# Kernel optimization log

Measured on AMD Instinct MI355X. Metric: run time of the kernel, lower is better.

Reference implementation:

```python
import jax, jax.numpy as jnp
import numpy as np

B, T, E, U, H = 1024, 200, 64, 64, 4  # batch, hist_len, embed, num_units, head_num
NEG = -2.0**32 + 1  # padding value from the TF code
EPS = 1e-9


def setup_inputs() -> dict:
    key = jax.random.key(0)
    k1, k2, k3, k4 = jax.random.split(key, 4)
    input_info = jax.random.normal(k1, (B, T, E), dtype=jnp.float32)
    keys_length = jax.random.randint(k2, (B, 1), 1, T + 1)  # valid lengths in [1, T]
    W = jax.random.truncated_normal(k3, -2.0, 2.0, (E, 3 * U), dtype=jnp.float32) * 0.05
    W_output = jax.random.truncated_normal(k4, -2.0, 2.0, (U, U), dtype=jnp.float32) * 0.05
    gamma = jnp.ones((U,), dtype=jnp.float32)
    beta = jnp.zeros((U,), dtype=jnp.float32)
    return {"input_info": input_info, "keys_length": keys_length,
            "W": W, "W_output": W_output, "gamma": gamma, "beta": beta}


def reference(input_info, keys_length, W, W_output, gamma, beta):
    b, t, e = input_info.shape
    u = W_output.shape[0]
    dh = u // H  # per-head dim; TF scales by sqrt of this (post-split dim)
    qkv = input_info @ W                     # [B,T,3U]
    q, k, v = jnp.split(qkv, 3, axis=-1)     # each [B,T,U]
    q = q.reshape(b, t, H, dh)
    k = k.reshape(b, t, H, dh)
    v = v.reshape(b, t, H, dh)
    scores = jnp.einsum('bqhd,bkhd->bhqk', q, k) / jnp.sqrt(jnp.float32(dh))
    mask = jnp.arange(t)[None, :] < keys_length          # [B,T] key mask
    scores = jnp.where(mask[:, None, None, :], scores, jnp.float32(NEG))
    align = jax.nn.softmax(scores, axis=-1)              # [B,H,T,T]
    out = jnp.einsum('bhqk,bkhd->bqhd', align, v).reshape(b, t, u)
    out = out @ W_output                                 # output projection
    out = out + input_info                               # residual (dropout off at inference)
    mean = out.mean(axis=-1, keepdims=True)
    var = jnp.mean((out - mean) ** 2, axis=-1, keepdims=True)
    out = (out - mean) / jnp.sqrt(var + EPS) * gamma + beta  # layernorm
    return out
```

## Files before the change

### kernel.cpp

```cpp
#include <hip/hip_runtime.h>

#define B_  1024
#define T_  200
#define E_  64
#define U_  64
#define H_  4

typedef float f32x4   __attribute__((ext_vector_type(4)));
typedef float f32x16  __attribute__((ext_vector_type(16)));
typedef short bf16x8  __attribute__((ext_vector_type(8)));
typedef unsigned uint2v __attribute__((ext_vector_type(2)));

static __device__ __forceinline__ float bf2f(unsigned short u) {
  return __uint_as_float(((unsigned)u) << 16);
}
static __device__ __forceinline__ float ldf(const void* p, long i, bool bf) {
  return bf ? bf2f(reinterpret_cast<const unsigned short*>(p)[i])
            : reinterpret_cast<const float*>(p)[i];
}
static __device__ __forceinline__ unsigned pkbf2(float lo, float hi) {
  unsigned r;
  asm("v_cvt_pk_bf16_f32 %0, %1, %2" : "=v"(r) : "v"(lo), "v"(hi));
  return r;
}
static __device__ __forceinline__ void swap32(unsigned& a, unsigned& b) {
#if defined(__has_builtin) && __has_builtin(__builtin_amdgcn_permlane32_swap)
  uint2v r = __builtin_amdgcn_permlane32_swap(a, b, false, false);
  a = r[0]; b = r[1];
#else
  asm volatile("v_permlane32_swap_b32 %0, %1" : "+v"(a), "+v"(b));
#endif
}

#define QK_IDX(t, c) ((((t) << 4) + (c)) ^ ((((t) >> 2) & 1) << 3))

__global__ __launch_bounds__(512, 4)
void mha_mfma(const void* __restrict__ input,
              const void* __restrict__ keys_length,
              const void* __restrict__ W,
              const void* __restrict__ Wo,
              const void* __restrict__ gamma,
              const void* __restrict__ beta,
              float* __restrict__ out) {
  __shared__ __align__(16) short sQ[224 * 16];
  __shared__ __align__(16) short sK[224 * 16];
  __shared__ __align__(16) short sVt[16 * 232];
  __shared__ __align__(16) short sWt[48 * 72];
  __shared__ __align__(16) short sWoT[64 * 72];
  __shared__ __align__(16) short sO[7 * 32 * 16];
  __shared__ float sGB[128];

  const int b    = blockIdx.x;
  const int tid  = threadIdx.x;
  const int wave = tid >> 6, lane = tid & 63;
  const int lane15 = lane & 15, quad = lane >> 4;
  const int lane31 = lane & 31, h5   = lane >> 5;

  const bool bf = (reinterpret_cast<const unsigned*>(gamma)[0] != 0x3F800000u);

  const unsigned* klu = reinterpret_cast<const unsigned*>(keys_length);
  const unsigned probe = klu[1];
  int len;
  if (probe == 0u)        len = (int)klu[2 * b];
  else if (probe <= 200u) len = (int)klu[b];
  else                    len = (int)__uint_as_float(klu[b]);
  len = len < 1 ? 1 : (len > T_ ? T_ : len);
  const int ntiles = (len + 31) >> 5;
  const int kvt16  = ntiles * 2;
  const int njobs  = 14 + 2 * kvt16;

  for (int i = tid; i < 64 * 64; i += 512) {
    int c = i & 63, r = i >> 6;
    sWoT[c * 72 + r] = (short)pkbf2(ldf(Wo, (long)r * 64 + c, bf), 0.f);
  }
  if (tid < 128) sGB[tid] = (tid < 64) ? ldf(gamma, tid, bf) : ldf(beta, tid - 64, bf);

  f32x16 oA, oB;
#pragma unroll
  for (int i = 0; i < 16; ++i) { oA[i] = 0.f; oB[i] = 0.f; }

  const int m32 = wave;
  const float* inpf = (const float*)input;

  for (int h = 0; h < H_; ++h) {
    for (int i = tid; i < 48 * 64; i += 512) {
      int jj = i % 48, e = i / 48;
      int col = (jj >> 4) * 64 + h * 16 + (jj & 15);
      sWt[jj * 72 + e] = (short)pkbf2(ldf(W, (long)e * 192 + col, bf), 0.f);
    }
    __syncthreads();

    for (int job = wave; job < njobs; job += 8) {
      int nn, m16;
      if (job < 14)              { nn = 0; m16 = job; }
      else if (job < 14 + kvt16) { nn = 1; m16 = job - 14; }
      else                       { nn = 2; m16 = job - 14 - kvt16; }
      int tg = m16 * 16 + lane15; if (tg > 199) tg = 199;
      bf16x8 a0, a1;
      unsigned* au0 = reinterpret_cast<unsigned*>(&a0);
      unsigned* au1 = reinterpret_cast<unsigned*>(&a1);
      if (!bf) {
        const float* rp = inpf + ((size_t)b * T_ + tg) * E_ + quad * 8;
        float4 u0 = *(const float4*)(rp);
        float4 v0 = *(const float4*)(rp + 4);
        float4 u1 = *(const float4*)(rp + 32);
        float4 v1 = *(const float4*)(rp + 36);
        au0[0] = pkbf2(u0.x, u0.y); au0[1] = pkbf2(u0.z, u0.w);
        au0[2] = pkbf2(v0.x, v0.y); au0[3] = pkbf2(v0.z, v0.w);
        au1[0] = pkbf2(u1.x, u1.y); au1[1] = pkbf2(u1.z, u1.w);
        au1[2] = pkbf2(v1.x, v1.y); au1[3] = pkbf2(v1.z, v1.w);
      } else {
        float af[16];
#pragma unroll
        for (int kh = 0; kh < 2; ++kh)
#pragma unroll
          for (int j = 0; j < 8; ++j)
            af[kh * 8 + j] = ldf(input, ((long)b * T_ + tg) * E_ + kh * 32 + quad * 8 + j, true);
#pragma unroll
        for (int j = 0; j < 4; ++j) au0[j] = pkbf2(af[2 * j], af[2 * j + 1]);
#pragma unroll
        for (int j = 0; j < 4; ++j) au1[j] = pkbf2(af[8 + 2 * j], af[8 + 2 * j + 1]);
      }
      bf16x8 b0 = *(const bf16x8*)&sWt[(nn * 16 + lane15) * 72 + quad * 8];
      bf16x8 b1 = *(const bf16x8*)&sWt[(nn * 16 + lane15) * 72 + 32 + quad * 8];
      f32x4 acc; acc[0] = 0.f; acc[1] = 0.f; acc[2] = 0.f; acc[3] = 0.f;
      acc = __builtin_amdgcn_mfma_f32_16x16x32_bf16(a0, b0, acc, 0, 0, 0);
      acc = __builtin_amdgcn_mfma_f32_16x16x32_bf16(a1, b1, acc, 0, 0, 0);
      const int tr = m16 * 16 + quad * 4;
      if (nn == 0) {
        const float qs = 0.36067376f;
        unsigned w01 = pkbf2(acc[0] * qs, acc[1] * qs);
        unsigned w23 = pkbf2(acc[2] * qs, acc[3] * qs);
        sQ[QK_IDX(tr + 0, lane15)] = (short)w01;
        sQ[QK_IDX(tr + 1, lane15)] = (short)(w01 >> 16);
        sQ[QK_IDX(tr + 2, lane15)] = (short)w23;
        sQ[QK_IDX(tr + 3, lane15)] = (short)(w23 >> 16);
      } else if (nn == 1) {
        unsigned w01 = pkbf2(acc[0], acc[1]);
        unsigned w23 = pkbf2(acc[2], acc[3]);
        sK[QK_IDX(tr + 0, lane15)] = (short)w01;
        sK[QK_IDX(tr + 1, lane15)] = (short)(w01 >> 16);
        sK[QK_IDX(tr + 2, lane15)] = (short)w23;
        sK[QK_IDX(tr + 3, lane15)] = (short)(w23 >> 16);
      } else {
        unsigned w01 = pkbf2(acc[0], acc[1]);
        unsigned w23 = pkbf2(acc[2], acc[3]);
        unsigned* vp = reinterpret_cast<unsigned*>(&sVt[lane15 * 232 + tr]);
        vp[0] = w01; vp[1] = w23;
      }
    }
    __syncthreads();

    if (m32 < 7) {
      bf16x8 qa = *(const bf16x8*)&sQ[QK_IDX(m32 * 32 + lane31, h5 * 8)];
      f32x16 Oacc;
#pragma unroll
      for (int i = 0; i < 16; ++i) Oacc[i] = 0.f;
      float lacc = 0.f;

      for (int kt = 0; kt < ntiles; ++kt) {
        bf16x8 kb = *(const bf16x8*)&sK[QK_IDX(kt * 32 + lane31, h5 * 8)];
        f32x16 s;
#pragma unroll
        for (int i = 0; i < 16; ++i) s[i] = 0.f;
        s = __builtin_amdgcn_mfma_f32_32x32x16_bf16(kb, qa, s, 0, 0, 0);
        float p[16];
        if (kt * 32 + 32 <= len) {
#pragma unroll
          for (int i = 0; i < 16; ++i) { p[i] = exp2f(s[i]); lacc += p[i]; }
        } else {
#pragma unroll
          for (int i = 0; i < 16; ++i) {
            const int tk = kt * 32 + (i & 3) + 8 * (i >> 2) + 4 * h5;
            const float e = exp2f(s[i]);
            p[i] = (tk < len) ? e : 0.f;
            lacc += p[i];
          }
        }
#pragma unroll
        for (int ks = 0; ks < 2; ++ks) {
          unsigned c0 = pkbf2(p[8 * ks + 0], p[8 * ks + 1]);
          unsigned c1 = pkbf2(p[8 * ks + 2], p[8 * ks + 3]);
          unsigned c2 = pkbf2(p[8 * ks + 4], p[8 * ks + 5]);
          unsigned c3 = pkbf2(p[8 * ks + 6], p[8 * ks + 7]);
          swap32(c0, c2);
          swap32(c1, c3);
          bf16x8 pa;
          unsigned* pw = reinterpret_cast<unsigned*>(&pa);
          pw[0] = c0; pw[1] = c1; pw[2] = c2; pw[3] = c3;
          bf16x8 vb;
#pragma unroll
          for (int z = 0; z < 8; ++z) vb[z] = 0;
          if (lane31 < 16)
            vb = *(const bf16x8*)&sVt[lane31 * 232 + kt * 32 + ks * 16 + h5 * 8];
          Oacc = __builtin_amdgcn_mfma_f32_32x32x16_bf16(pa, vb, Oacc, 0, 0, 0);
        }
      }
      lacc += __shfl_xor(lacc, 32);
      const float rinv = 1.0f / lacc;
#pragma unroll
      for (int i = 0; i < 16; i += 2) {
        const int r0 = (i & 3) + 8 * (i >> 2) + 4 * h5;
        const unsigned w = pkbf2(Oacc[i], Oacc[i + 1]);
        if (lane31 < 16) {
          sO[(m32 << 9) + QK_IDX(r0,     lane31)] = (short)w;
          sO[(m32 << 9) + QK_IDX(r0 + 1, lane31)] = (short)(w >> 16);
        }
      }
      bf16x8 oraw = *(const bf16x8*)&sO[(m32 << 9) + QK_IDX(lane31, h5 * 8)];
      const unsigned* op = reinterpret_cast<const unsigned*>(&oraw);
      bf16x8 oa;
      unsigned* np = reinterpret_cast<unsigned*>(&oa);
#pragma unroll
      for (int j = 0; j < 4; ++j) {
        const float lo = __uint_as_float(op[j] << 16) * rinv;
        const float hi = __uint_as_float(op[j] & 0xffff0000u) * rinv;
        np[j] = pkbf2(lo, hi);
      }
      bf16x8 w0 = *(const bf16x8*)&sWoT[lane31 * 72 + h * 16 + h5 * 8];
      bf16x8 w1 = *(const bf16x8*)&sWoT[(32 + lane31) * 72 + h * 16 + h5 * 8];
      oA = __builtin_amdgcn_mfma_f32_32x32x16_bf16(oa, w0, oA, 0, 0, 0);
      oB = __builtin_amdgcn_mfma_f32_32x32x16_bf16(oa, w1, oB, 0, 0, 0);
    }
  }

  if (m32 < 7) {
    const float g0 = sGB[lane31], g1 = sGB[32 + lane31];
    const float be0 = sGB[64 + lane31], be1 = sGB[96 + lane31];
#pragma unroll
    for (int i = 0; i < 16; ++i) {
      const int t = m32 * 32 + (i & 3) + 8 * (i >> 2) + 4 * h5;
      const bool valid = t < 200;
      const size_t base = ((size_t)b * T_ + t) * E_;
      float x0 = oA[i], x1 = oB[i];
      if (valid) {
        if (!bf) { x0 += inpf[base + lane31]; x1 += inpf[base + 32 + lane31]; }
        else     { x0 += ldf(input, base + lane31, true); x1 += ldf(input, base + 32 + lane31, true); }
      }
      float sx = x0 + x1, sxx = x0 * x0 + x1 * x1;
#pragma unroll
      for (int off = 1; off < 32; off <<= 1) {
        sx  += __shfl_xor(sx, off);
        sxx += __shfl_xor(sxx, off);
      }
      const float mean = sx * (1.0f / 64.0f);
      float var = sxx * (1.0f / 64.0f) - mean * mean;
      var = var < 0.f ? 0.f : var;
      const float inv = rsqrtf(var + 1e-9f);
      if (valid) {
        out[base + lane31]      = (x0 - mean) * inv * g0 + be0;
        out[base + 32 + lane31] = (x1 - mean) * inv * g1 + be1;
      }
    }
  }
}

static const void* pick_by_size(void* const* d_in, const int* in_sizes, int n_in,
                                int want, int which, const void* fallback) {
  int seen = 0;
  for (int i = 0; i < n_in; ++i) {
    if (in_sizes[i] == want) {
      if (seen == which) return d_in[i];
      ++seen;
    }
  }
  return fallback;
}

extern "C" void kernel_launch(void* const* d_in, const int* in_sizes, int n_in,
                              void* d_out, int out_size, void* d_ws, size_t ws_size,
                              hipStream_t stream) {
  const void* input  = pick_by_size(d_in, in_sizes, n_in, B_ * T_ * E_, 0, d_in[0]);
  const void* klen   = pick_by_size(d_in, in_sizes, n_in, B_,           0, d_in[1]);
  const void* W      = pick_by_size(d_in, in_sizes, n_in, E_ * 3 * U_,  0, d_in[2]);
  const void* Wo     = pick_by_size(d_in, in_sizes, n_in, U_ * U_,      0, d_in[3]);
  const void* gamma  = pick_by_size(d_in, in_sizes, n_in, U_,           0, d_in[4]);
  const void* beta   = pick_by_size(d_in, in_sizes, n_in, U_,           1, d_in[5]);
  float* o           = (float*)d_out;
  (void)out_size; (void)d_ws; (void)ws_size;
  mha_mfma<<<dim3(B_), dim3(512), 0, stream>>>(input, klen, W, Wo, gamma, beta, o);
}
```

Measured before the change: 234.0 us.

## Reuse input A-fragments across Q/K/V projections per wave, drop LDS swizzle

The QKV projection moves from a job queue, where each wave computed one of Q, K or V for one 16-row tile, to each wave owning two row tiles and computing all three projections from a single load and conversion of the input rows. This removes the triple global load and bf16 conversion of the input per head. It also drops the XOR swizzle on the Q/K layout, which may bring back LDS bank conflicts. It replaces the hardware pack-convert with a software round-to-nearest bf16 conversion and computes K/V for all rows instead of only up to the valid key length.

```diff
diff --git a/kernel.cpp b/kernel.cpp
--- a/kernel.cpp
+++ b/kernel.cpp
@@ -11,6 +11,11 @@
 typedef short bf16x8  __attribute__((ext_vector_type(8)));
 typedef unsigned uint2v __attribute__((ext_vector_type(2)));
 
+static __device__ __forceinline__ unsigned short f2bf(float x) {
+  unsigned u = __float_as_uint(x);
+  u += 0x7FFFu + ((u >> 16) & 1u);
+  return (unsigned short)(u >> 16);
+}
 static __device__ __forceinline__ float bf2f(unsigned short u) {
   return __uint_as_float(((unsigned)u) << 16);
 }
@@ -42,9 +47,9 @@
               const void* __restrict__ gamma,
               const void* __restrict__ beta,
               float* __restrict__ out) {
-  __shared__ __align__(16) short sQ[224 * 16];
-  __shared__ __align__(16) short sK[224 * 16];
-  __shared__ __align__(16) short sVt[16 * 232];
+  __shared__ __align__(16) short sQ[256 * 16];
+  __shared__ __align__(16) short sK[256 * 16];
+  __shared__ __align__(16) short sVt[16 * 264];
   __shared__ __align__(16) short sWt[48 * 72];
   __shared__ __align__(16) short sWoT[64 * 72];
   __shared__ __align__(16) short sO[7 * 32 * 16];
@@ -66,12 +71,10 @@
   else                    len = (int)__uint_as_float(klu[b]);
   len = len < 1 ? 1 : (len > T_ ? T_ : len);
   const int ntiles = (len + 31) >> 5;
-  const int kvt16  = ntiles * 2;
-  const int njobs  = 14 + 2 * kvt16;
 
   for (int i = tid; i < 64 * 64; i += 512) {
     int c = i & 63, r = i >> 6;
-    sWoT[c * 72 + r] = (short)pkbf2(ldf(Wo, (long)r * 64 + c, bf), 0.f);
+    sWoT[c * 72 + r] = (short)f2bf(ldf(Wo, (long)r * 64 + c, bf));
   }
   if (tid < 128) sGB[tid] = (tid < 64) ? ldf(gamma, tid, bf) : ldf(beta, tid - 64, bf);
 
@@ -86,80 +89,67 @@
     for (int i = tid; i < 48 * 64; i += 512) {
       int jj = i % 48, e = i / 48;
       int col = (jj >> 4) * 64 + h * 16 + (jj & 15);
-      sWt[jj * 72 + e] = (short)pkbf2(ldf(W, (long)e * 192 + col, bf), 0.f);
+      sWt[jj * 72 + e] = (short)f2bf(ldf(W, (long)e * 192 + col, bf));
     }
     __syncthreads();
 
-    for (int job = wave; job < njobs; job += 8) {
-      int nn, m16;
-      if (job < 14)              { nn = 0; m16 = job; }
-      else if (job < 14 + kvt16) { nn = 1; m16 = job - 14; }
-      else                       { nn = 2; m16 = job - 14 - kvt16; }
-      int tg = m16 * 16 + lane15; if (tg > 199) tg = 199;
-      bf16x8 a0, a1;
-      unsigned* au0 = reinterpret_cast<unsigned*>(&a0);
-      unsigned* au1 = reinterpret_cast<unsigned*>(&a1);
-      if (!bf) {
-        const float* rp = inpf + ((size_t)b * T_ + tg) * E_ + quad * 8;
-        float4 u0 = *(const float4*)(rp);
-        float4 v0 = *(const float4*)(rp + 4);
-        float4 u1 = *(const float4*)(rp + 32);
-        float4 v1 = *(const float4*)(rp + 36);
-        au0[0] = pkbf2(u0.x, u0.y); au0[1] = pkbf2(u0.z, u0.w);
-        au0[2] = pkbf2(v0.x, v0.y); au0[3] = pkbf2(v0.z, v0.w);
-        au1[0] = pkbf2(u1.x, u1.y); au1[1] = pkbf2(u1.z, u1.w);
-        au1[2] = pkbf2(v1.x, v1.y); au1[3] = pkbf2(v1.z, v1.w);
-      } else {
-        float af[16];
-#pragma unroll
-        for (int kh = 0; kh < 2; ++kh)
-#pragma unroll
-          for (int j = 0; j < 8; ++j)
-            af[kh * 8 + j] = ldf(input, ((long)b * T_ + tg) * E_ + kh * 32 + quad * 8 + j, true);
-#pragma unroll
-        for (int j = 0; j < 4; ++j) au0[j] = pkbf2(af[2 * j], af[2 * j + 1]);
-#pragma unroll
-        for (int j = 0; j < 4; ++j) au1[j] = pkbf2(af[8 + 2 * j], af[8 + 2 * j + 1]);
-      }
-      bf16x8 b0 = *(const bf16x8*)&sWt[(nn * 16 + lane15) * 72 + quad * 8];
-      bf16x8 b1 = *(const bf16x8*)&sWt[(nn * 16 + lane15) * 72 + 32 + quad * 8];
-      f32x4 acc; acc[0] = 0.f; acc[1] = 0.f; acc[2] = 0.f; acc[3] = 0.f;
-      acc = __builtin_amdgcn_mfma_f32_16x16x32_bf16(a0, b0, acc, 0, 0, 0);
-      acc = __builtin_amdgcn_mfma_f32_16x16x32_bf16(a1, b1, acc, 0, 0, 0);
-      const int tr = m16 * 16 + quad * 4;
-      if (nn == 0) {
-        const float qs = 0.36067376f;
-        unsigned w01 = pkbf2(acc[0] * qs, acc[1] * qs);
-        unsigned w23 = pkbf2(acc[2] * qs, acc[3] * qs);
-        sQ[QK_IDX(tr + 0, lane15)] = (short)w01;
-        sQ[QK_IDX(tr + 1, lane15)] = (short)(w01 >> 16);
-        sQ[QK_IDX(tr + 2, lane15)] = (short)w23;
-        sQ[QK_IDX(tr + 3, lane15)] = (short)(w23 >> 16);
-      } else if (nn == 1) {
-        unsigned w01 = pkbf2(acc[0], acc[1]);
-        unsigned w23 = pkbf2(acc[2], acc[3]);
-        sK[QK_IDX(tr + 0, lane15)] = (short)w01;
-        sK[QK_IDX(tr + 1, lane15)] = (short)(w01 >> 16);
-        sK[QK_IDX(tr + 2, lane15)] = (short)w23;
-        sK[QK_IDX(tr + 3, lane15)] = (short)(w23 >> 16);
-      } else {
-        unsigned w01 = pkbf2(acc[0], acc[1]);
-        unsigned w23 = pkbf2(acc[2], acc[3]);
-        unsigned* vp = reinterpret_cast<unsigned*>(&sVt[lane15 * 232 + tr]);
-        vp[0] = w01; vp[1] = w23;
+#pragma unroll
+    for (int mi = 0; mi < 2; ++mi) {
+      const int m16 = wave * 2 + mi;
+      if (m16 < 14) {
+        int tg = m16 * 16 + lane15; if (tg > 199) tg = 199;
+        float af[2][8];
+        if (!bf) {
+          const float* rp = inpf + ((size_t)b * T_ + tg) * E_;
+#pragma unroll
+          for (int kh = 0; kh < 2; ++kh) {
+            float4 u = *(const float4*)(rp + kh * 32 + quad * 8);
+            float4 v = *(const float4*)(rp + kh * 32 + quad * 8 + 4);
+            af[kh][0] = u.x; af[kh][1] = u.y; af[kh][2] = u.z; af[kh][3] = u.w;
+            af[kh][4] = v.x; af[kh][5] = v.y; af[kh][6] = v.z; af[kh][7] = v.w;
+          }
+        } else {
+#pragma unroll
+          for (int kh = 0; kh < 2; ++kh)
+#pragma unroll
+            for (int j = 0; j < 8; ++j)
+              af[kh][j] = ldf(input, ((long)b * T_ + tg) * E_ + kh * 32 + quad * 8 + j, true);
+        }
+        bf16x8 a0, a1;
+#pragma unroll
+        for (int j = 0; j < 8; ++j) { a0[j] = (short)f2bf(af[0][j]); a1[j] = (short)f2bf(af[1][j]); }
+#pragma unroll
+        for (int nn = 0; nn < 3; ++nn) {
+          bf16x8 b0 = *(const bf16x8*)&sWt[(nn * 16 + lane15) * 72 + quad * 8];
+          bf16x8 b1 = *(const bf16x8*)&sWt[(nn * 16 + lane15) * 72 + 32 + quad * 8];
+          f32x4 acc; acc[0] = 0.f; acc[1] = 0.f; acc[2] = 0.f; acc[3] = 0.f;
+          acc = __builtin_amdgcn_mfma_f32_16x16x32_bf16(a0, b0, acc, 0, 0, 0);
+          acc = __builtin_amdgcn_mfma_f32_16x16x32_bf16(a1, b1, acc, 0, 0, 0);
+          const int tr = m16 * 16 + quad * 4;
+          if (nn == 0) {
+#pragma unroll
+            for (int r = 0; r < 4; ++r) sQ[(tr + r) * 16 + lane15] = (short)f2bf(acc[r] * 0.36067376f);
+          } else if (nn == 1) {
+#pragma unroll
+            for (int r = 0; r < 4; ++r) sK[(tr + r) * 16 + lane15] = (short)f2bf(acc[r]);
+          } else {
+#pragma unroll
+            for (int r = 0; r < 4; ++r) sVt[lane15 * 264 + tr + r] = (short)f2bf(acc[r]);
+          }
+        }
       }
     }
     __syncthreads();
 
     if (m32 < 7) {
-      bf16x8 qa = *(const bf16x8*)&sQ[QK_IDX(m32 * 32 + lane31, h5 * 8)];
+      bf16x8 qa = *(const bf16x8*)&sQ[(m32 * 32 + lane31) * 16 + h5 * 8];
       f32x16 Oacc;
 #pragma unroll
       for (int i = 0; i < 16; ++i) Oacc[i] = 0.f;
       float lacc = 0.f;
 
       for (int kt = 0; kt < ntiles; ++kt) {
-        bf16x8 kb = *(const bf16x8*)&sK[QK_IDX(kt * 32 + lane31, h5 * 8)];
+        bf16x8 kb = *(const bf16x8*)&sK[(kt * 32 + lane31) * 16 + h5 * 8];
         f32x16 s;
 #pragma unroll
         for (int i = 0; i < 16; ++i) s[i] = 0.f;
@@ -192,7 +182,7 @@
 #pragma unroll
           for (int z = 0; z < 8; ++z) vb[z] = 0;
           if (lane31 < 16)
-            vb = *(const bf16x8*)&sVt[lane31 * 232 + kt * 32 + ks * 16 + h5 * 8];
+            vb = *(const bf16x8*)&sVt[lane31 * 264 + kt * 32 + ks * 16 + h5 * 8];
           Oacc = __builtin_amdgcn_mfma_f32_32x32x16_bf16(pa, vb, Oacc, 0, 0, 0);
         }
       }
```

Measured after the change: 214.2 us. 1.09x faster.
